# Performance work log

Measured on AMD Instinct MI355X. Metric: run time of the kernel, lower is better.

The kernel has to match this reference:

```python
import jax, jax.numpy as jnp
import numpy as np

B, S, D = 2, 2048, 768
H, DK, F = 12, 64, 3072
LN_EPS = 1e-5


def setup_inputs() -> dict:
    key = jax.random.key(0)
    ks = jax.random.split(key, 8)
    w = lambda k, shape: jax.random.normal(k, shape, dtype=jnp.float32) * 0.02
    return {
        "x": jax.random.normal(ks[0], (B, S, D), dtype=jnp.float32),
        "wq_w": w(ks[1], (H, D, DK)), "wq_b": jnp.zeros((H, DK), jnp.float32),
        "wk_w": w(ks[2], (H, D, DK)), "wk_b": jnp.zeros((H, DK), jnp.float32),
        "wv_w": w(ks[3], (H, D, DK)), "wv_b": jnp.zeros((H, DK), jnp.float32),
        "wo_w": w(ks[4], (H * DK, D)), "wo_b": jnp.zeros((D,), jnp.float32),
        "ln_g": jnp.ones((D,), jnp.float32), "ln_b": jnp.zeros((D,), jnp.float32),
        "w1": w(ks[5], (D, F)), "b1": jnp.zeros((F,), jnp.float32),
        "w2": w(ks[6], (F, D)), "b2": jnp.zeros((D,), jnp.float32),
    }


def layer_norm(x, g, b):
    mu = jnp.mean(x, axis=-1, keepdims=True)
    var = jnp.mean(jnp.square(x - mu), axis=-1, keepdims=True)
    return (x - mu) * jax.lax.rsqrt(var + LN_EPS) * g + b


def reference(x, wq_w, wq_b, wk_w, wk_b, wv_w, wv_b, wo_w, wo_b,
              ln_g, ln_b, w1, b1, w2, b2):
    dk = wq_w.shape[-1]
    x_res = x
    h = layer_norm(x, ln_b=ln_b, g=ln_g, b=ln_b) if False else layer_norm(x, ln_g, ln_b)
    # per-head QKV (all heads batched via einsum): [B,H,S,DK]
    q = jnp.einsum("bsd,hdk->bhsk", h, wq_w) + wq_b[None, :, None, :]
    k = jnp.einsum("bsd,hdk->bhsk", h, wk_w) + wk_b[None, :, None, :]
    v = jnp.einsum("bsd,hdk->bhsk", h, wv_w) + wv_b[None, :, None, :]
    scores = jnp.einsum("bhqk,bhsk->bhqs", q, k) / jnp.sqrt(jnp.float32(dk))
    attn = jax.nn.softmax(scores, axis=-1)
    o = jnp.einsum("bhqs,bhsk->bhqk", attn, v)  # [B,H,S,DK]
    Bx, Hx, Sx, Dkx = o.shape
    o = o.transpose(0, 2, 1, 3).reshape(Bx, Sx, Hx * Dkx)  # concat heads
    y = o @ wo_w + wo_b + x_res  # residual 1
    y_res = y
    z = layer_norm(y, ln_g, ln_b)
    z = jax.nn.gelu(z @ w1 + b1, approximate=False) @ w2 + b2
    return z + y_res
```

## Files before the change

kernel.cpp:

```cpp
#include <hip/hip_runtime.h>
#include <hip/hip_bf16.h>
#include <math.h>

typedef __bf16 bf16_t;
typedef __bf16 bf16x8 __attribute__((ext_vector_type(8)));
typedef __bf16 bf16x4 __attribute__((ext_vector_type(4)));
typedef float f32x4 __attribute__((ext_vector_type(4)));

#define MFMA_B16(a, b, c) __builtin_amdgcn_mfma_f32_16x16x32_bf16((a), (b), (c), 0, 0, 0)

static constexpr int Bn = 2, Sn = 2048, Dn = 768, Hn = 12, Fn = 3072;
static constexpr int NTOK = Bn * Sn;
#define QSCALE 0.18033688011112042f

__device__ __forceinline__ void gl_lds16(const bf16_t* g, void* lds) {
  __builtin_amdgcn_global_load_lds(
      (const __attribute__((address_space(1))) uint32_t*)g,
      (__attribute__((address_space(3))) uint32_t*)lds, 16, 0, 0);
}

__global__ __launch_bounds__(256) void k_prep(const float* __restrict__ wq, const float* __restrict__ wk,
                                              const float* __restrict__ wv, const float* __restrict__ wo,
                                              const float* __restrict__ w1, const float* __restrict__ w2,
                                              const float* __restrict__ bq, const float* __restrict__ bk,
                                              const float* __restrict__ bv,
                                              bf16_t* __restrict__ WqkvT, bf16_t* __restrict__ WoT,
                                              bf16_t* __restrict__ W1T, bf16_t* __restrict__ W2T,
                                              float* __restrict__ QKVB,
                                              const float* __restrict__ x, const float* __restrict__ ln_g,
                                              const float* __restrict__ ln_b, bf16_t* __restrict__ Hbuf) {
  int t = blockIdx.x;
  int tid = threadIdx.x;
  if (t >= 1729) {
    int tok = t - 1729;
    const float* xr = x + (size_t)tok * Dn;
    float v0 = xr[tid], v1 = xr[tid + 256], v2 = xr[tid + 512];
    float s = v0 + v1 + v2;
    float ss = v0 * v0 + v1 * v1 + v2 * v2;
    __shared__ float red[8];
#pragma unroll
    for (int off = 32; off > 0; off >>= 1) {
      s += __shfl_down(s, off);
      ss += __shfl_down(ss, off);
    }
    int w = tid >> 6, l = tid & 63;
    if (l == 0) { red[w] = s; red[4 + w] = ss; }
    __syncthreads();
    s = red[0] + red[1] + red[2] + red[3];
    ss = red[4] + red[5] + red[6] + red[7];
    float mu = s * (1.0f / Dn);
    float var = ss * (1.0f / Dn) - mu * mu;
    float rstd = rsqrtf(var + 1e-5f);
    bf16_t* orow = Hbuf + (size_t)tok * Dn;
    orow[tid]       = (bf16_t)((v0 - mu) * rstd * ln_g[tid]       + ln_b[tid]);
    orow[tid + 256] = (bf16_t)((v1 - mu) * rstd * ln_g[tid + 256] + ln_b[tid + 256]);
    orow[tid + 512] = (bf16_t)((v2 - mu) * rstd * ln_g[tid + 512] + ln_b[tid + 512]);
    return;
  }
  if (t == 1728) {
    for (int i = tid; i < 2304; i += 256)
      QKVB[i] = i < 768 ? bq[i] : (i < 1536 ? bk[i - 768] : bv[i - 1536]);
    return;
  }
  __shared__ float T[64][65];
  const float* src;
  bf16_t* dst;
  int P, Q, tp, tq;
  if (t < 432) {
    int pb = t / 12; tp = t - pb * 12; tq = 0;
    int proj = pb / 12, head = pb - proj * 12;
    src = (proj == 0 ? wq : proj == 1 ? wk : wv) + (size_t)head * 768 * 64;
    dst = WqkvT + (size_t)proj * 589824 + (size_t)head * 64 * 768;
    P = 768; Q = 64;
  } else if (t < 576) {
    int u = t - 432; tp = u / 12; tq = u - tp * 12;
    src = wo; dst = WoT; P = 768; Q = 768;
  } else if (t < 1152) {
    int u = t - 576; tp = u / 48; tq = u - tp * 48;
    src = w1; dst = W1T; P = 768; Q = 3072;
  } else {
    int u = t - 1152; tp = u / 12; tq = u - tp * 12;
    src = w2; dst = W2T; P = 3072; Q = 768;
  }
  int j = tid & 63, i0 = tid >> 6;
#pragma unroll
  for (int i = i0; i < 64; i += 4)
    T[i][j] = src[(size_t)(tp * 64 + i) * Q + tq * 64 + j];
  __syncthreads();
#pragma unroll
  for (int i = i0; i < 64; i += 4)
    dst[(size_t)(tq * 64 + i) * P + tp * 64 + j] = (bf16_t)T[j][i];
}

__global__ __launch_bounds__(256) void k_layernorm(const float* __restrict__ x,
                                                   const float* __restrict__ g,
                                                   const float* __restrict__ bb,
                                                   bf16_t* __restrict__ out) {
  int t = blockIdx.x, tid = threadIdx.x;
  const float* xr = x + (size_t)t * Dn;
  float v0 = xr[tid], v1 = xr[tid + 256], v2 = xr[tid + 512];
  float s = v0 + v1 + v2;
  float ss = v0 * v0 + v1 * v1 + v2 * v2;
  __shared__ float red[8];
#pragma unroll
  for (int off = 32; off > 0; off >>= 1) {
    s += __shfl_down(s, off);
    ss += __shfl_down(ss, off);
  }
  int w = tid >> 6, l = tid & 63;
  if (l == 0) { red[w] = s; red[4 + w] = ss; }
  __syncthreads();
  s = red[0] + red[1] + red[2] + red[3];
  ss = red[4] + red[5] + red[6] + red[7];
  float mu = s * (1.0f / Dn);
  float var = ss * (1.0f / Dn) - mu * mu;
  float rstd = rsqrtf(var + 1e-5f);
  bf16_t* orow = out + (size_t)t * Dn;
  orow[tid]       = (bf16_t)((v0 - mu) * rstd * g[tid]       + bb[tid]);
  orow[tid + 256] = (bf16_t)((v1 - mu) * rstd * g[tid + 256] + bb[tid + 256]);
  orow[tid + 512] = (bf16_t)((v2 - mu) * rstd * g[tid + 512] + bb[tid + 512]);
}

enum { EPI_QK = 0, EPI_VT = 1, EPI_Y = 2, EPI_GELU = 3, EPI_OUT = 4 };

template <int MT, int NT, int BK, int EPI, int OCC, int SWZ>
__global__ __launch_bounds__(256, OCC) void k_gemm(const bf16_t* __restrict__ A,
                                                   const bf16_t* __restrict__ Bt,
                                                   int N, int K,
                                                   const float* __restrict__ bias,
                                                   const float* __restrict__ resid,
                                                   void* __restrict__ out0,
                                                   void* __restrict__ out1) {
  constexpr int MI = MT / 32, NI = NT / 32;
  constexpr int WROWS = MT / 2, WCOLS = NT / 2;
  constexpr int KS = BK / 32;
  __shared__ __align__(16) bf16_t As[2][MT * BK];
  __shared__ __align__(16) bf16_t Bs[2][NT * BK];
  const int tid = threadIdx.x;
  const int w = tid >> 6, l = tid & 63;
  const int wm = w >> 1, wn = w & 1;
  const int mloc = l & 15, kblk = l >> 4;
  int bx = blockIdx.x, by = blockIdx.y;
  if constexpr (SWZ) {
    int lin = by * gridDim.x + bx;
    int xcd = lin & 7, s = lin >> 3;
    by = xcd * (gridDim.y >> 3) + s / gridDim.x;
    bx = s - (s / gridDim.x) * gridDim.x;
  }

  f32x4 acc[MI][NI];
#pragma unroll
  for (int i = 0; i < MI; ++i)
#pragma unroll
    for (int j = 0; j < NI; ++j) acc[i][j] = f32x4{0.f, 0.f, 0.f, 0.f};

  const bf16_t* gA = A + (size_t)(by * MT + (tid >> 2)) * K + (tid & 3) * 8;
  const bf16_t* gB = Bt + (size_t)(bx * NT + (tid >> 2)) * K + (tid & 3) * 8;
  const int nk = K / BK;

  auto stage = [&](int kt, int buf) {
#pragma unroll
    for (int h = 0; h < KS; ++h) {
#pragma unroll
      for (int rb = 0; rb < MT / 64; ++rb)
        gl_lds16(gA + (size_t)rb * 64 * K + kt * BK + h * 32,
                 (char*)&As[buf][0] + h * (MT * 64) + rb * 4096 + w * 1024);
#pragma unroll
      for (int rb = 0; rb < NT / 64; ++rb)
        gl_lds16(gB + (size_t)rb * 64 * K + kt * BK + h * 32,
                 (char*)&Bs[buf][0] + h * (NT * 64) + rb * 4096 + w * 1024);
    }
  };

  stage(0, 0);
  for (int kt = 0; kt < nk; ++kt) {
    __syncthreads();
    if (kt + 1 < nk) stage(kt + 1, (kt + 1) & 1);
    const bf16_t* Ab = &As[kt & 1][0];
    const bf16_t* Bb = &Bs[kt & 1][0];
    bf16x8 af[MI][KS], bfv[NI][KS];
#pragma unroll
    for (int mi = 0; mi < MI; ++mi)
#pragma unroll
      for (int ks = 0; ks < KS; ++ks)
        af[mi][ks] = *(const bf16x8*)&Ab[ks * (MT * 32) + (wm * WROWS + mi * 16 + mloc) * 32 + kblk * 8];
#pragma unroll
    for (int ni = 0; ni < NI; ++ni)
#pragma unroll
      for (int ks = 0; ks < KS; ++ks)
        bfv[ni][ks] = *(const bf16x8*)&Bb[ks * (NT * 32) + (wn * WCOLS + ni * 16 + mloc) * 32 + kblk * 8];
#pragma unroll
    for (int ks = 0; ks < KS; ++ks)
#pragma unroll
      for (int mi = 0; mi < MI; ++mi)
#pragma unroll
        for (int ni = 0; ni < NI; ++ni)
          acc[mi][ni] = MFMA_B16(af[mi][ks], bfv[ni][ks], acc[mi][ni]);
  }

  const int gmb = by * MT + wm * WROWS + kblk * 4;
  const int gnb = bx * NT + wn * WCOLS + mloc;
  if constexpr (EPI == EPI_QK) {
    constexpr int TPP = 768 / NT;
    const int proj = bx / TPP;
#pragma unroll
    for (int mi = 0; mi < MI; ++mi)
#pragma unroll
      for (int ni = 0; ni < NI; ++ni) {
        int gn = gnb + ni * 16;
        float bv = bias[gn];
        int gm0 = gmb + mi * 16;
        if (proj == 0) {
          bf16_t* dst = (bf16_t*)out0;
#pragma unroll
          for (int r = 0; r < 4; ++r)
            dst[(size_t)(gm0 + r) * 768 + gn] = (bf16_t)((acc[mi][ni][r] + bv) * QSCALE);
        } else {
          bf16_t* dst = (bf16_t*)out1;
#pragma unroll
          for (int r = 0; r < 4; ++r)
            dst[(size_t)(gm0 + r) * 768 + (gn - 768)] = (bf16_t)(acc[mi][ni][r] + bv);
        }
      }
  } else if constexpr (EPI == EPI_VT) {
    bf16_t* dst = (bf16_t*)out0;
#pragma unroll
    for (int mi = 0; mi < MI; ++mi)
#pragma unroll
      for (int ni = 0; ni < NI; ++ni) {
        int gn = gnb + ni * 16;
        int bq = gn >> 11, sq = gn & 2047;
#pragma unroll
        for (int r = 0; r < 4; ++r) {
          int gm = gmb + mi * 16 + r;
          int hq = gm >> 6, dk = gm & 63;
          dst[((size_t)(bq * Hn + hq) * 64 + dk) * Sn + sq] = (bf16_t)(acc[mi][ni][r] + bias[gm]);
        }
      }
  } else if constexpr (EPI == EPI_GELU) {
    bf16_t* dst = (bf16_t*)out0;
#pragma unroll
    for (int mi = 0; mi < MI; ++mi)
#pragma unroll
      for (int ni = 0; ni < NI; ++ni) {
        int gn = gnb + ni * 16;
        float bv = bias[gn];
#pragma unroll
        for (int r = 0; r < 4; ++r) {
          int gm = gmb + mi * 16 + r;
          float t = acc[mi][ni][r] + bv;
          float ge = 0.5f * t * (1.0f + erff(t * 0.70710678118654752f));
          dst[(size_t)gm * N + gn] = (bf16_t)ge;
        }
      }
  } else {
    float* dst = (float*)out0;
#pragma unroll
    for (int mi = 0; mi < MI; ++mi)
#pragma unroll
      for (int ni = 0; ni < NI; ++ni) {
        int gn = gnb + ni * 16;
        float bv = bias[gn];
#pragma unroll
        for (int r = 0; r < 4; ++r) {
          int gm = gmb + mi * 16 + r;
          dst[(size_t)gm * N + gn] = acc[mi][ni][r] + bv + resid[(size_t)gm * N + gn];
        }
      }
  }
}

__global__ __launch_bounds__(256, 2) void k_attn(const bf16_t* __restrict__ Q,
                                                 const bf16_t* __restrict__ K,
                                                 const bf16_t* __restrict__ VT,
                                                 bf16_t* __restrict__ O) {
  __shared__ __align__(16) bf16_t Ks[2][8192];
  __shared__ __align__(16) bf16_t Vs[2][8192];
  const int tid = threadIdx.x, w = tid >> 6, l = tid & 63;
  const int mloc = l & 15, kblk = l >> 4;
  const int bh = blockIdx.y, b = bh / Hn, h = bh - b * Hn;
  const int q0 = blockIdx.x * 128;

  const size_t qoffA = (size_t)(b * Sn + q0 + w * 32 + mloc) * Dn + h * 64 + kblk * 8;
  const bf16x8 qfa0 = *(const bf16x8*)(Q + qoffA);
  const bf16x8 qfa1 = *(const bf16x8*)(Q + qoffA + 32);
  const bf16x8 qfb0 = *(const bf16x8*)(Q + qoffA + (size_t)16 * Dn);
  const bf16x8 qfb1 = *(const bf16x8*)(Q + qoffA + (size_t)16 * Dn + 32);

  bf16x8 ones;
#pragma unroll
  for (int j = 0; j < 8; ++j) ones[j] = (bf16_t)1.0f;

  const int tq = tid >> 2, q4 = tid & 3;
  const int s0 = (tq & 0x20) | ((tq & 0x0C) << 1) | ((tq & 0x10) >> 2) | (tq & 3);
  const bf16_t* Kg = K + (size_t)(b * Sn + s0) * Dn + h * 64 + q4 * 8;
  const bf16_t* Vg = VT + ((size_t)bh * 64 + (l >> 2)) * Sn + w * 32 + (l & 3) * 8;

  f32x4 lacca = f32x4{0.f, 0.f, 0.f, 0.f};
  f32x4 laccb = f32x4{0.f, 0.f, 0.f, 0.f};
  f32x4 oacca[4], oaccb[4];
#pragma unroll
  for (int md = 0; md < 4; ++md) {
    oacca[md] = f32x4{0.f, 0.f, 0.f, 0.f};
    oaccb[md] = f32x4{0.f, 0.f, 0.f, 0.f};
  }

  auto stage = [&](int kv0, int buf) {
#pragma unroll
    for (int rb = 0; rb < 2; ++rb)
#pragma unroll
      for (int hh = 0; hh < 2; ++hh)
        gl_lds16(Kg + (size_t)(kv0 + rb * 64) * Dn + hh * 32,
                 (char*)&Ks[buf][0] + hh * 8192 + rb * 4096 + w * 1024);
#pragma unroll
    for (int j = 0; j < 4; ++j)
      gl_lds16(Vg + kv0 + (size_t)j * 16 * Sn,
               (char*)&Vs[buf][0] + w * 4096 + j * 1024);
  };

  stage(0, 0);
  for (int it = 0; it < Sn / 128; ++it) {
    __syncthreads();
    if (it + 1 < Sn / 128) stage((it + 1) * 128, (it + 1) & 1);
    const bf16_t* Kb = &Ks[it & 1][0];
    const bf16_t* Vb = &Vs[it & 1][0];

    f32x4 sa[8], sb[8];
#pragma unroll
    for (int ns = 0; ns < 8; ++ns) {
      const bf16x8 k0 = *(const bf16x8*)&Kb[(ns * 16 + mloc) * 32 + kblk * 8];
      const bf16x8 k1 = *(const bf16x8*)&Kb[4096 + (ns * 16 + mloc) * 32 + kblk * 8];
      f32x4 a = f32x4{0.f, 0.f, 0.f, 0.f};
      a = MFMA_B16(k0, qfa0, a);
      a = MFMA_B16(k1, qfa1, a);
      sa[ns] = a;
      f32x4 c = f32x4{0.f, 0.f, 0.f, 0.f};
      c = MFMA_B16(k0, qfb0, c);
      c = MFMA_B16(k1, qfb1, c);
      sb[ns] = c;
    }

    bf16x8 pa[4], pbv[4];
#pragma unroll
    for (int ns = 0; ns < 8; ++ns)
#pragma unroll
      for (int r = 0; r < 4; ++r) {
        pa[ns >> 1][(ns & 1) * 4 + r]  = (bf16_t)__builtin_amdgcn_exp2f(sa[ns][r]);
        pbv[ns >> 1][(ns & 1) * 4 + r] = (bf16_t)__builtin_amdgcn_exp2f(sb[ns][r]);
      }

#pragma unroll
    for (int c = 0; c < 4; ++c) {
      lacca = MFMA_B16(ones, pa[c], lacca);
      laccb = MFMA_B16(ones, pbv[c], laccb);
    }

#pragma unroll
    for (int md = 0; md < 4; ++md)
#pragma unroll
      for (int c = 0; c < 4; ++c) {
        const bf16x8 v = *(const bf16x8*)&Vb[c * 2048 + (md * 16 + mloc) * 32 + kblk * 8];
        oacca[md] = MFMA_B16(v, pa[c], oacca[md]);
        oaccb[md] = MFMA_B16(v, pbv[c], oaccb[md]);
      }
  }

  const float invA = 1.0f / lacca[0];
  const float invB = 1.0f / laccb[0];
  const size_t obA = (size_t)(b * Sn + q0 + w * 32 + mloc) * Dn + h * 64 + kblk * 4;
  const size_t obB = obA + (size_t)16 * Dn;
#pragma unroll
  for (int md = 0; md < 4; ++md) {
    bf16x4 oa, ob;
#pragma unroll
    for (int r = 0; r < 4; ++r) {
      oa[r] = (bf16_t)(oacca[md][r] * invA);
      ob[r] = (bf16_t)(oaccb[md][r] * invB);
    }
    *(bf16x4*)&O[obA + md * 16] = oa;
    *(bf16x4*)&O[obB + md * 16] = ob;
  }
}

extern "C" void kernel_launch(void* const* d_in, const int* in_sizes, int n_in,
                              void* d_out, int out_size, void* d_ws, size_t ws_size,
                              hipStream_t stream) {
  (void)in_sizes; (void)n_in; (void)out_size; (void)ws_size;
  const float* x    = (const float*)d_in[0];
  const float* wq_w = (const float*)d_in[1];
  const float* wq_b = (const float*)d_in[2];
  const float* wk_w = (const float*)d_in[3];
  const float* wk_b = (const float*)d_in[4];
  const float* wv_w = (const float*)d_in[5];
  const float* wv_b = (const float*)d_in[6];
  const float* wo_w = (const float*)d_in[7];
  const float* wo_b = (const float*)d_in[8];
  const float* ln_g = (const float*)d_in[9];
  const float* ln_b = (const float*)d_in[10];
  const float* w1   = (const float*)d_in[11];
  const float* b1   = (const float*)d_in[12];
  const float* w2   = (const float*)d_in[13];
  const float* b2   = (const float*)d_in[14];

  char* ws = (char*)d_ws;
  size_t o = 0;
  bf16_t* WqkvT = (bf16_t*)(ws + o); o += (size_t)2304 * 768 * 2;
  bf16_t* WoT   = (bf16_t*)(ws + o); o += (size_t)768 * 768 * 2;
  bf16_t* W1T   = (bf16_t*)(ws + o); o += (size_t)3072 * 768 * 2;
  bf16_t* W2T   = (bf16_t*)(ws + o); o += (size_t)768 * 3072 * 2;
  float*  QKVB  = (float*)(ws + o);  o += (size_t)2304 * 4;
  bf16_t* Hbuf  = (bf16_t*)(ws + o); o += (size_t)NTOK * 768 * 2;
  bf16_t* Qb    = (bf16_t*)(ws + o); o += (size_t)NTOK * 768 * 2;
  bf16_t* Kb    = (bf16_t*)(ws + o); o += (size_t)NTOK * 768 * 2;
  bf16_t* VbT   = (bf16_t*)(ws + o); o += (size_t)NTOK * 768 * 2;
  float*  Ybuf  = (float*)(ws + o);  o += (size_t)NTOK * 768 * 4;
  bf16_t* Zbuf  = (bf16_t*)(ws + o); o += (size_t)NTOK * 768 * 2;
  bf16_t* Ubuf  = (bf16_t*)(ws + o); o += (size_t)NTOK * 3072 * 2;

  k_prep<<<1729 + NTOK, 256, 0, stream>>>(wq_w, wk_w, wv_w, wo_w, w1, w2,
                                          wq_b, wk_b, wv_b, WqkvT, WoT, W1T, W2T, QKVB,
                                          x, ln_g, ln_b, Hbuf);

  k_gemm<128, 64, 64, EPI_QK, 3, 1><<<dim3(24, 32), 256, 0, stream>>>(Hbuf, WqkvT, 1536, 768,
                                                                      QKVB, nullptr, Qb, Kb);

  k_gemm<64, 64, 64, EPI_VT, 4, 0><<<dim3(64, 12), 256, 0, stream>>>(WqkvT + (size_t)2 * 589824, Hbuf,
                                                                     4096, 768, QKVB + 1536, nullptr,
                                                                     VbT, nullptr);

  k_attn<<<dim3(Sn / 128, Bn * Hn), 256, 0, stream>>>(Qb, Kb, VbT, Hbuf);

  k_gemm<64, 64, 64, EPI_Y, 4, 1><<<dim3(12, 64), 256, 0, stream>>>(Hbuf, WoT, 768, 768,
                                                                    wo_b, x, Ybuf, nullptr);

  k_layernorm<<<NTOK, 256, 0, stream>>>(Ybuf, ln_g, ln_b, Zbuf);

  k_gemm<128, 128, 32, EPI_GELU, 3, 1><<<dim3(24, 32), 256, 0, stream>>>(Zbuf, W1T, 3072, 768,
                                                                         b1, nullptr, Ubuf, nullptr);

  k_gemm<64, 64, 64, EPI_OUT, 4, 1><<<dim3(12, 64), 256, 0, stream>>>(Ubuf, W2T, 768, 3072,
                                                                      b2, Ybuf, d_out, nullptr);
}
```

Before: 267.9 us.

## Split attention KV loop across two wave groups with LDS reduction

The attention kernel now launches 512 threads per block: two groups of four waves each process alternating 64-key tiles for the same 128 queries, then the second group writes its partial O and row sums to LDS and the first group adds them and stores the output. This doubles the waves available per block to hide latency in the KV loop without extra global traffic for Q. In exchange it adds a final LDS reduction and extra barriers, and the larger blocks may lower how many blocks fit per CU given the 64KB LDS footprint.

```diff
diff --git a/kernel.cpp b/kernel.cpp
--- a/kernel.cpp
+++ b/kernel.cpp
@@ -270,18 +270,18 @@
   }
 }
 
-__global__ __launch_bounds__(256, 2) void k_attn(const bf16_t* __restrict__ Q,
+__global__ __launch_bounds__(512, 2) void k_attn(const bf16_t* __restrict__ Q,
                                                  const bf16_t* __restrict__ K,
                                                  const bf16_t* __restrict__ VT,
                                                  bf16_t* __restrict__ O) {
-  __shared__ __align__(16) bf16_t Ks[2][8192];
-  __shared__ __align__(16) bf16_t Vs[2][8192];
+  __shared__ __align__(16) char smem[65536];
   const int tid = threadIdx.x, w = tid >> 6, l = tid & 63;
+  const int g = w >> 2, lw = w & 3;
   const int mloc = l & 15, kblk = l >> 4;
   const int bh = blockIdx.y, b = bh / Hn, h = bh - b * Hn;
   const int q0 = blockIdx.x * 128;
 
-  const size_t qoffA = (size_t)(b * Sn + q0 + w * 32 + mloc) * Dn + h * 64 + kblk * 8;
+  const size_t qoffA = (size_t)(b * Sn + q0 + lw * 32 + mloc) * Dn + h * 64 + kblk * 8;
   const bf16x8 qfa0 = *(const bf16x8*)(Q + qoffA);
   const bf16x8 qfa1 = *(const bf16x8*)(Q + qoffA + 32);
   const bf16x8 qfb0 = *(const bf16x8*)(Q + qoffA + (size_t)16 * Dn);
@@ -291,10 +291,16 @@
 #pragma unroll
   for (int j = 0; j < 8; ++j) ones[j] = (bf16_t)1.0f;
 
-  const int tq = tid >> 2, q4 = tid & 3;
-  const int s0 = (tq & 0x20) | ((tq & 0x0C) << 1) | ((tq & 0x10) >> 2) | (tq & 3);
-  const bf16_t* Kg = K + (size_t)(b * Sn + s0) * Dn + h * 64 + q4 * 8;
-  const bf16_t* Vg = VT + ((size_t)bh * 64 + (l >> 2)) * Sn + w * 32 + (l & 3) * 8;
+  const int tq = lw * 16 + (l >> 2);
+  const int s0 = (tq & 0x23) | ((tq & 0x0C) << 1) | ((tq & 0x10) >> 2);
+  const bf16_t* Kg = K + (size_t)(b * Sn + s0) * Dn + h * 64 + (l & 3) * 8;
+  const int c0 = (2 * lw) >> 2, rg0 = (2 * lw) & 3;
+  const int c1 = (2 * lw + 1) >> 2, rg1 = (2 * lw + 1) & 3;
+  const bf16_t* Vg0 = VT + ((size_t)bh * 64 + rg0 * 16 + (l >> 2)) * Sn + c0 * 32 + (l & 3) * 8;
+  const bf16_t* Vg1 = VT + ((size_t)bh * 64 + rg1 * 16 + (l >> 2)) * Sn + c1 * 32 + (l & 3) * 8;
+
+  char* Kbase = smem + g * 16384;
+  char* Vbase = smem + 32768 + g * 16384;
 
   f32x4 lacca = f32x4{0.f, 0.f, 0.f, 0.f};
   f32x4 laccb = f32x4{0.f, 0.f, 0.f, 0.f};
@@ -305,31 +311,27 @@
     oaccb[md] = f32x4{0.f, 0.f, 0.f, 0.f};
   }
 
-  auto stage = [&](int kv0, int buf) {
-#pragma unroll
-    for (int rb = 0; rb < 2; ++rb)
-#pragma unroll
-      for (int hh = 0; hh < 2; ++hh)
-        gl_lds16(Kg + (size_t)(kv0 + rb * 64) * Dn + hh * 32,
-                 (char*)&Ks[buf][0] + hh * 8192 + rb * 4096 + w * 1024);
-#pragma unroll
-    for (int j = 0; j < 4; ++j)
-      gl_lds16(Vg + kv0 + (size_t)j * 16 * Sn,
-               (char*)&Vs[buf][0] + w * 4096 + j * 1024);
+  auto stage = [&](int tile, int buf) {
+    const size_t kv0 = (size_t)tile * 64;
+    gl_lds16(Kg + kv0 * Dn,      Kbase + buf * 8192 + lw * 1024);
+    gl_lds16(Kg + kv0 * Dn + 32, Kbase + buf * 8192 + 4096 + lw * 1024);
+    gl_lds16(Vg0 + kv0, Vbase + buf * 8192 + c0 * 4096 + rg0 * 1024);
+    gl_lds16(Vg1 + kv0, Vbase + buf * 8192 + c1 * 4096 + rg1 * 1024);
   };
 
-  stage(0, 0);
-  for (int it = 0; it < Sn / 128; ++it) {
+  constexpr int NIT = Sn / 128;
+  stage(g, 0);
+  for (int ii = 0; ii < NIT; ++ii) {
     __syncthreads();
-    if (it + 1 < Sn / 128) stage((it + 1) * 128, (it + 1) & 1);
-    const bf16_t* Kb = &Ks[it & 1][0];
-    const bf16_t* Vb = &Vs[it & 1][0];
-
-    f32x4 sa[8], sb[8];
-#pragma unroll
-    for (int ns = 0; ns < 8; ++ns) {
+    if (ii + 1 < NIT) stage(g + 2 * (ii + 1), (ii + 1) & 1);
+    const bf16_t* Kb = (const bf16_t*)(Kbase + (ii & 1) * 8192);
+    const bf16_t* Vb = (const bf16_t*)(Vbase + (ii & 1) * 8192);
+
+    f32x4 sa[4], sb[4];
+#pragma unroll
+    for (int ns = 0; ns < 4; ++ns) {
       const bf16x8 k0 = *(const bf16x8*)&Kb[(ns * 16 + mloc) * 32 + kblk * 8];
-      const bf16x8 k1 = *(const bf16x8*)&Kb[4096 + (ns * 16 + mloc) * 32 + kblk * 8];
+      const bf16x8 k1 = *(const bf16x8*)&Kb[2048 + (ns * 16 + mloc) * 32 + kblk * 8];
       f32x4 a = f32x4{0.f, 0.f, 0.f, 0.f};
       a = MFMA_B16(k0, qfa0, a);
       a = MFMA_B16(k1, qfa1, a);
@@ -340,9 +342,9 @@
       sb[ns] = c;
     }
 
-    bf16x8 pa[4], pbv[4];
-#pragma unroll
-    for (int ns = 0; ns < 8; ++ns)
+    bf16x8 pa[2], pbv[2];
+#pragma unroll
+    for (int ns = 0; ns < 4; ++ns)
 #pragma unroll
       for (int r = 0; r < 4; ++r) {
         pa[ns >> 1][(ns & 1) * 4 + r]  = (bf16_t)__builtin_amdgcn_exp2f(sa[ns][r]);
@@ -350,7 +352,7 @@
       }
 
 #pragma unroll
-    for (int c = 0; c < 4; ++c) {
+    for (int c = 0; c < 2; ++c) {
       lacca = MFMA_B16(ones, pa[c], lacca);
       laccb = MFMA_B16(ones, pbv[c], laccb);
     }
@@ -358,27 +360,51 @@
 #pragma unroll
     for (int md = 0; md < 4; ++md)
 #pragma unroll
-      for (int c = 0; c < 4; ++c) {
+      for (int c = 0; c < 2; ++c) {
         const bf16x8 v = *(const bf16x8*)&Vb[c * 2048 + (md * 16 + mloc) * 32 + kblk * 8];
         oacca[md] = MFMA_B16(v, pa[c], oacca[md]);
         oaccb[md] = MFMA_B16(v, pbv[c], oaccb[md]);
       }
   }
 
-  const float invA = 1.0f / lacca[0];
-  const float invB = 1.0f / laccb[0];
-  const size_t obA = (size_t)(b * Sn + q0 + w * 32 + mloc) * Dn + h * 64 + kblk * 4;
-  const size_t obB = obA + (size_t)16 * Dn;
-#pragma unroll
-  for (int md = 0; md < 4; ++md) {
-    bf16x4 oa, ob;
-#pragma unroll
-    for (int r = 0; r < 4; ++r) {
-      oa[r] = (bf16_t)(oacca[md][r] * invA);
-      ob[r] = (bf16_t)(oaccb[md][r] * invB);
+  __syncthreads();
+  float* Red = (float*)smem;
+  float* p = Red + (size_t)(lw * 64 + l) * 34;
+  if (g == 1) {
+#pragma unroll
+    for (int md = 0; md < 4; ++md)
+#pragma unroll
+      for (int r = 0; r < 4; ++r) {
+        p[md * 4 + r]      = oacca[md][r];
+        p[16 + md * 4 + r] = oaccb[md][r];
+      }
+    p[32] = lacca[0];
+    p[33] = laccb[0];
+  }
+  __syncthreads();
+  if (g == 0) {
+#pragma unroll
+    for (int md = 0; md < 4; ++md)
+#pragma unroll
+      for (int r = 0; r < 4; ++r) {
+        oacca[md][r] += p[md * 4 + r];
+        oaccb[md][r] += p[16 + md * 4 + r];
+      }
+    const float invA = 1.0f / (lacca[0] + p[32]);
+    const float invB = 1.0f / (laccb[0] + p[33]);
+    const size_t obA = (size_t)(b * Sn + q0 + lw * 32 + mloc) * Dn + h * 64 + kblk * 4;
+    const size_t obB = obA + (size_t)16 * Dn;
+#pragma unroll
+    for (int md = 0; md < 4; ++md) {
+      bf16x4 oa, ob;
+#pragma unroll
+      for (int r = 0; r < 4; ++r) {
+        oa[r] = (bf16_t)(oacca[md][r] * invA);
+        ob[r] = (bf16_t)(oaccb[md][r] * invB);
+      }
+      *(bf16x4*)&O[obA + md * 16] = oa;
+      *(bf16x4*)&O[obB + md * 16] = ob;
     }
-    *(bf16x4*)&O[obA + md * 16] = oa;
-    *(bf16x4*)&O[obB + md * 16] = ob;
   }
 }
 
@@ -428,7 +454,7 @@
                                                                      4096, 768, QKVB + 1536, nullptr,
                                                                      VbT, nullptr);
 
-  k_attn<<<dim3(Sn / 128, Bn * Hn), 256, 0, stream>>>(Qb, Kb, VbT, Hbuf);
+  k_attn<<<dim3(Sn / 128, Bn * Hn), 512, 0, stream>>>(Qb, Kb, VbT, Hbuf);
 
   k_gemm<64, 64, 64, EPI_Y, 4, 1><<<dim3(12, 64), 256, 0, stream>>>(Hbuf, WoT, 768, 768,
                                                                     wo_b, x, Ybuf, nullptr);
```

Result: no change. 265.6 us (-0.9%).
